# Kernel tuning notes

Hardware: AMD Instinct MI355X
Metric: run time of the kernel (lower is better)

The kernel has to match this reference:

```python
import jax, jax.numpy as jnp
import numpy as np

B = 64  # number of graph pairs in the batch


def gcn_conv(x, W, b, edge_index, n_nodes):
    """PyG GCNConv: add self-loops, symmetric deg^-1/2 normalization, x@W then aggregate."""
    h = x @ W  # [N, out]
    src = jnp.concatenate([edge_index[0], jnp.arange(n_nodes)])
    dst = jnp.concatenate([edge_index[1], jnp.arange(n_nodes)])
    deg = jax.ops.segment_sum(jnp.ones_like(dst, dtype=h.dtype), dst, num_segments=n_nodes)
    dinv = jnp.where(deg > 0, jax.lax.rsqrt(jnp.maximum(deg, 1e-12)), 0.0)
    coef = dinv[src] * dinv[dst]  # [E+N]
    out = jax.ops.segment_sum(coef[:, None] * h[src], dst, num_segments=n_nodes)
    return out + b


def mean_pool(x, batch, num_graphs):
    sums = jax.ops.segment_sum(x, batch, num_segments=num_graphs)
    cnts = jax.ops.segment_sum(jnp.ones((x.shape[0],), x.dtype), batch, num_segments=num_graphs)
    return sums / jnp.maximum(cnts, 1.0)[:, None]


def setup_inputs() -> dict:
    key = jax.random.key(0)
    ks = jax.random.split(key, 32)
    n_prot, e_prot, n_mol, e_mol = 100000, 1600000, 4096, 16384

    def lin(k, fin, fout):
        k1, k2 = jax.random.split(k)
        s = 1.0 / np.sqrt(fin)
        return (jax.random.uniform(k1, (fin, fout), jnp.float32, -s, s),
                jax.random.uniform(k2, (fout,), jnp.float32, -s, s))

    fc1_w, fc1_b = lin(ks[0], 18640, 128)
    fc2_w, fc2_b = lin(ks[1], 128, 128)
    fcm1_w, fcm1_b = lin(ks[2], 21, 64)
    fcm2_w, fcm2_b = lin(ks[3], 64, 64)
    gp1_w, gp1_b = lin(ks[4], 9, 128)
    gp2_w, gp2_b = lin(ks[5], 128, 128)
    gm1_w, gm1_b = lin(ks[6], 9, 128)
    gm2_w, gm2_b = lin(ks[7], 128, 128)
    fcc_w, fcc_b = lin(ks[8], 448, 128)
    out_w, out_b = lin(ks[9], 128, 2)

    return {
        "metadata_prot": jax.random.normal(ks[10], (B, 18640), jnp.float32),
        "metadata_mol": jax.random.normal(ks[11], (B, 21), jnp.float32),
        "x_prot": jax.random.normal(ks[12], (n_prot, 9), jnp.float32),
        "x_mol": jax.random.normal(ks[13], (n_mol, 9), jnp.float32),
        "edge_index_prot": jax.random.randint(ks[14], (2, e_prot), 0, n_prot),
        "batch_vector_prot": jnp.sort(jax.random.randint(ks[15], (n_prot,), 0, B)),
        "edge_index_mol": jax.random.randint(ks[16], (2, e_mol), 0, n_mol),
        "batch_vector_mol": jnp.sort(jax.random.randint(ks[17], (n_mol,), 0, B)),
        "fc1_w": fc1_w, "fc1_b": fc1_b, "fc2_w": fc2_w, "fc2_b": fc2_b,
        "fcm1_w": fcm1_w, "fcm1_b": fcm1_b, "fcm2_w": fcm2_w, "fcm2_b": fcm2_b,
        "gp1_w": gp1_w, "gp1_b": gp1_b, "gp2_w": gp2_w, "gp2_b": gp2_b,
        "gm1_w": gm1_w, "gm1_b": gm1_b, "gm2_w": gm2_w, "gm2_b": gm2_b,
        "fcc_w": fcc_w, "fcc_b": fcc_b, "out_w": out_w, "out_b": out_b,
    }


def reference(metadata_prot, metadata_mol, x_prot, x_mol,
              edge_index_prot, batch_vector_prot, edge_index_mol, batch_vector_mol,
              fc1_w, fc1_b, fc2_w, fc2_b, fcm1_w, fcm1_b, fcm2_w, fcm2_b,
              gp1_w, gp1_b, gp2_w, gp2_b, gm1_w, gm1_b, gm2_w, gm2_b,
              fcc_w, fcc_b, out_w, out_b):
    relu = jax.nn.relu
    mp = relu(relu(metadata_prot @ fc1_w + fc1_b) @ fc2_w + fc2_b)
    mm = relu(relu(metadata_mol @ fcm1_w + fcm1_b) @ fcm2_w + fcm2_b)

    n_prot = x_prot.shape[0]
    hp = relu(gcn_conv(x_prot, gp1_w, gp1_b, edge_index_prot, n_prot))
    hp = relu(gcn_conv(hp, gp2_w, gp2_b, edge_index_prot, n_prot))
    hp = mean_pool(hp, batch_vector_prot, B)

    n_mol = x_mol.shape[0]
    hm = relu(gcn_conv(x_mol, gm1_w, gm1_b, edge_index_mol, n_mol))
    hm = relu(gcn_conv(hm, gm2_w, gm2_b, edge_index_mol, n_mol))
    hm = mean_pool(hm, batch_vector_mol, B)

    combined = jnp.concatenate([mp, mm, hp, hm], axis=1)  # [B, 448]
    combined = relu(combined @ fcc_w + fcc_b)
    return relu(combined @ out_w + out_b)  # [B, 2]
```

## Files before the change

### kernel.cpp

```cpp
#include <hip/hip_runtime.h>

#define CAP 64
#define GB  64
#define FC1K 18640
#define CH 932
#define KS 20
#define NRP 8

typedef __attribute__((ext_vector_type(8))) short bf16x8;
typedef __attribute__((ext_vector_type(4))) float f32x4;

static inline int cdiv(long a, long b){ return (int)((a + b - 1) / b); }

__device__ inline unsigned short pack_bf1(float a) {
  unsigned ua = __float_as_uint(a); ua += 0x7fffu + ((ua >> 16) & 1u);
  return (unsigned short)(ua >> 16);
}
__device__ inline unsigned pack_bf2(float a, float b) {
  unsigned ua = __float_as_uint(a); ua += 0x7fffu + ((ua >> 16) & 1u);
  unsigned ub = __float_as_uint(b); ub += 0x7fffu + ((ub >> 16) & 1u);
  return (ua >> 16) | (ub & 0xffff0000u);
}
__device__ inline float unpack_lo(unsigned short u) { return __uint_as_float(((unsigned)u) << 16); }

__global__ void k_mega(const float* __restrict__ md, const float* __restrict__ fc1w,
                       float* __restrict__ part,
                       const int* __restrict__ ei_m, int EM,
                       int* __restrict__ cnt_m, int* __restrict__ idx_m, int MOLB,
                       const int* __restrict__ bv_p, int NP,
                       const int* __restrict__ bv_m, int NM,
                       float* __restrict__ cntp, float* __restrict__ cntm,
                       const int* __restrict__ ei_p, int EP, int step,
                       int* __restrict__ cnt_p, int* __restrict__ idx_p) {
  __shared__ float smd[64][KS];
  int bid = blockIdx.x;
  int tid = threadIdx.x;

  if (bid < CH) {
    int c = bid;
    int k0 = c * KS;
    for (int t = tid; t < 64 * KS; t += 256) {
      int b = t / KS, k = t % KS;
      smd[b][k] = md[(size_t)b * FC1K + k0 + k];
    }
    __syncthreads();
    int j = tid & 127, bg = tid >> 7;
    float acc[32];
    #pragma unroll
    for (int i = 0; i < 32; i++) acc[i] = 0.f;
    for (int k = 0; k < KS; k++) {
      float w = fc1w[(size_t)(k0 + k) * 128 + j];
      #pragma unroll
      for (int i = 0; i < 32; i++) acc[i] += smd[bg * 32 + i][k] * w;
    }
    float* dst = part + ((size_t)c * 64 + bg * 32) * 128 + j;
    #pragma unroll
    for (int i = 0; i < 32; i++) dst[(size_t)i * 128] = acc[i];
    return;
  }
  bid -= CH;

  if (bid < MOLB) {
    int e = bid * 256 + tid;
    if (e < EM) {
      int s = ei_m[e], d = ei_m[EM + e];
      int c = atomicAdd(&cnt_m[d], 1);
      if (c < CAP) idx_m[d * CAP + c] = s;
    }
    return;
  }
  bid -= MOLB;

  if (bid == 0) {
    if (tid < 128) {
      const int* batch; float* cnt; int n, b;
      if (tid < 64) { batch = bv_p; n = NP; cnt = cntp; b = tid; }
      else          { batch = bv_m; n = NM; cnt = cntm; b = tid - 64; }
      int lo = 0, hi = n;
      while (lo < hi) { int mid = (lo + hi) >> 1; if (batch[mid] < b) lo = mid + 1; else hi = mid; }
      int start = lo;
      lo = 0; hi = n;
      while (lo < hi) { int mid = (lo + hi) >> 1; if (batch[mid] <= b) lo = mid + 1; else hi = mid; }
      cnt[b] = (float)(lo - start);
    }
    return;
  }
  bid -= 1;

  {
    int r = bid & 7;
    int lo = r * step, hi = lo + step; if (hi > NP) hi = NP;
    long eb = (long)(bid >> 3) * 1024 + tid;
    int d0 = -1, d1 = -1, d2 = -1, d3 = -1;
    if (eb       < EP) d0 = ei_p[EP + eb];
    if (eb + 256 < EP) d1 = ei_p[EP + eb + 256];
    if (eb + 512 < EP) d2 = ei_p[EP + eb + 512];
    if (eb + 768 < EP) d3 = ei_p[EP + eb + 768];
    bool a0 = (d0 >= lo) & (d0 < hi);
    bool a1 = (d1 >= lo) & (d1 < hi);
    bool a2 = (d2 >= lo) & (d2 < hi);
    bool a3 = (d3 >= lo) & (d3 < hi);
    int s0 = a0 ? ei_p[eb]       : 0;
    int s1 = a1 ? ei_p[eb + 256] : 0;
    int s2 = a2 ? ei_p[eb + 512] : 0;
    int s3 = a3 ? ei_p[eb + 768] : 0;
    if (a0) { int c = atomicAdd(&cnt_p[d0], 1); if (c < CAP) idx_p[d0 * CAP + c] = s0; }
    if (a1) { int c = atomicAdd(&cnt_p[d1], 1); if (c < CAP) idx_p[d1 * CAP + c] = s1; }
    if (a2) { int c = atomicAdd(&cnt_p[d2], 1); if (c < CAP) idx_p[d2 * CAP + c] = s2; }
    if (a3) { int c = atomicAdd(&cnt_p[d3], 1); if (c < CAP) idx_p[d3 * CAP + c] = s3; }
  }
}

__global__ void k_prep(const float* __restrict__ part, const float* __restrict__ b1,
                       const float* __restrict__ W2, const float* __restrict__ b2,
                       float* __restrict__ mp,
                       const int* __restrict__ cnt_p, const float* __restrict__ x_p,
                       float* __restrict__ dinv_p, unsigned short* __restrict__ xs_p, int np,
                       const int* __restrict__ cnt_m, const float* __restrict__ x_m,
                       float* __restrict__ dinv_m, unsigned short* __restrict__ xs_m, int nm) {
  __shared__ float red[8][128];
  __shared__ float row[128];
  int bid = blockIdx.x, tid = threadIdx.x;
  if (bid < GB) {
    int b = bid;
    int j = tid & 127, kg = tid >> 7;
    float acc = 0.f;
    #pragma unroll 4
    for (int c = kg; c < CH; c += 8) acc += part[((size_t)c * 64 + b) * 128 + j];
    red[kg][j] = acc;
    __syncthreads();
    if (kg == 0) {
      float s = red[0][j] + red[1][j] + red[2][j] + red[3][j]
              + red[4][j] + red[5][j] + red[6][j] + red[7][j];
      row[j] = fmaxf(s + b1[j], 0.f);
    }
    __syncthreads();
    float a2 = 0.f;
    int k0 = kg * 16;
    #pragma unroll
    for (int k = k0; k < k0 + 16; k++) a2 += row[k] * W2[k * 128 + j];
    red[kg][j] = a2;
    __syncthreads();
    if (kg == 0) {
      float s = red[0][j] + red[1][j] + red[2][j] + red[3][j]
              + red[4][j] + red[5][j] + red[6][j] + red[7][j];
      mp[b * 128 + j] = fmaxf(s + b2[j], 0.f);
    }
    return;
  }
  long t = (long)(bid - GB) * 1024 + tid;
  const int* cnt; const float* x; float* dinv; unsigned short* xs; int v, f;
  long tp = (long)np * 16;
  if (t < tp) { v = (int)(t >> 4); f = (int)(t & 15); cnt = cnt_p; x = x_p; dinv = dinv_p; xs = xs_p; }
  else {
    t -= tp;
    if (t >= (long)nm * 16) return;
    v = (int)(t >> 4); f = (int)(t & 15); cnt = cnt_m; x = x_m; dinv = dinv_m; xs = xs_m;
  }
  float d = rsqrtf((float)cnt[v] + 1.0f);
  if (f == 0) dinv[v] = d;
  xs[(size_t)v * 16 + f] = (f < 9) ? pack_bf1(d * x[(size_t)v * 9 + f]) : (unsigned short)0;
}

__global__ void k_gcn1(const unsigned short* __restrict__ xs_p, const float* __restrict__ dinv_p,
                       const int* __restrict__ cnt_p, const int* __restrict__ idx_p,
                       const float* __restrict__ W1p, const float* __restrict__ b1p,
                       const float* __restrict__ W2p, unsigned* __restrict__ hout_p, int np,
                       const unsigned short* __restrict__ xs_m, const float* __restrict__ dinv_m,
                       const int* __restrict__ cnt_m, const int* __restrict__ idx_m,
                       const float* __restrict__ W1m, const float* __restrict__ b1m,
                       const float* __restrict__ W2m, unsigned* __restrict__ hout_m, int nm,
                       int PB) {
  __shared__ float W1s[9 * 128];
  __shared__ float b1s[128];
  __shared__ float axs[16][16];
  __shared__ uint4 As4[256];
  const unsigned short* xs; const float* dinv; const int* cnt; const int* idx;
  const float* W1; const float* b1; const float* W2; unsigned* hout; int n, tile0, gsz;
  if ((int)blockIdx.x < PB) {
    xs = xs_p; dinv = dinv_p; cnt = cnt_p; idx = idx_p;
    W1 = W1p; b1 = b1p; W2 = W2p; hout = hout_p; n = np;
    tile0 = blockIdx.x; gsz = PB;
  } else {
    xs = xs_m; dinv = dinv_m; cnt = cnt_m; idx = idx_m;
    W1 = W1m; b1 = b1m; W2 = W2m; hout = hout_m; n = nm;
    tile0 = blockIdx.x - PB; gsz = gridDim.x - PB;
  }
  int ntiles = (n + 15) >> 4;
  int tid = threadIdx.x;
  int lane = tid & 63;
  int wave = tid >> 6;
  int l15 = lane & 15;
  int lg  = lane >> 4;

  for (int i = tid; i < 9 * 128; i += 256) W1s[i] = W1[i];
  if (tid < 128) b1s[tid] = b1[tid];

  bf16x8 bfrag[2][4];
  #pragma unroll
  for (int ct = 0; ct < 2; ct++) {
    int col = wave * 32 + ct * 16 + l15;
    #pragma unroll
    for (int ks = 0; ks < 4; ks++) {
      #pragma unroll
      for (int j = 0; j < 8; j++) {
        int k = ks * 32 + lg * 8 + j;
        bfrag[ct][ks][j] = (short)pack_bf1(W2[(size_t)k * 128 + col]);
      }
    }
  }
  __syncthreads();

  int r = tid >> 4, c4 = tid & 15;
  for (int tile = tile0; tile < ntiles; tile += gsz) {
    int base = tile * 16;
    int v = base + r;
    float acc = 0.f;
    if (v < n) {
      int deg = cnt[v]; if (deg > CAP) deg = CAP;
      const int* idxv = idx + (size_t)v * CAP;
      acc = unpack_lo(xs[(size_t)v * 16 + c4]);
      int p = 0;
      for (; p + 4 <= deg; p += 4) {
        int s0 = idxv[p], s1 = idxv[p + 1], s2 = idxv[p + 2], s3 = idxv[p + 3];
        float a0 = unpack_lo(xs[(size_t)s0 * 16 + c4]);
        float a1 = unpack_lo(xs[(size_t)s1 * 16 + c4]);
        float a2 = unpack_lo(xs[(size_t)s2 * 16 + c4]);
        float a3 = unpack_lo(xs[(size_t)s3 * 16 + c4]);
        acc += a0; acc += a1; acc += a2; acc += a3;
      }
      for (; p < deg; p++) acc += unpack_lo(xs[(size_t)idxv[p] * 16 + c4]);
      acc *= dinv[v];
    }
    axs[r][c4] = acc;
    __syncthreads();

    float h[8];
    int j0 = c4 * 8;
    #pragma unroll
    for (int jj = 0; jj < 8; jj++) h[jj] = b1s[j0 + jj];
    #pragma unroll
    for (int k = 0; k < 9; k++) {
      float a = axs[r][k];
      #pragma unroll
      for (int jj = 0; jj < 8; jj++) h[jj] += a * W1s[k * 128 + j0 + jj];
    }
    uint4 av;
    av.x = pack_bf2(fmaxf(h[0], 0.f), fmaxf(h[1], 0.f));
    av.y = pack_bf2(fmaxf(h[2], 0.f), fmaxf(h[3], 0.f));
    av.z = pack_bf2(fmaxf(h[4], 0.f), fmaxf(h[5], 0.f));
    av.w = pack_bf2(fmaxf(h[6], 0.f), fmaxf(h[7], 0.f));
    As4[r * 16 + (c4 ^ r)] = av;
    __syncthreads();

    bf16x8 afr[4];
    #pragma unroll
    for (int ks = 0; ks < 4; ks++) {
      uint4 a4 = As4[l15 * 16 + (((ks * 4) + lg) ^ l15)];
      afr[ks] = *(bf16x8*)&a4;
    }

    f32x4 acc0 = {0.f, 0.f, 0.f, 0.f}, acc1 = {0.f, 0.f, 0.f, 0.f};
    #pragma unroll
    for (int ks = 0; ks < 4; ks++) {
      acc0 = __builtin_amdgcn_mfma_f32_16x16x32_bf16(afr[ks], bfrag[0][ks], acc0, 0, 0, 0);
      acc1 = __builtin_amdgcn_mfma_f32_16x16x32_bf16(afr[ks], bfrag[1][ks], acc1, 0, 0, 0);
    }

    #pragma unroll
    for (int reg = 0; reg < 4; reg++) {
      int row = lg * 4 + reg;
      int ov = base + row;
      if (ov < n) {
        float dv = dinv[ov];
        unsigned short* hp16 = (unsigned short*)hout;
        hp16[(size_t)ov * 128 + wave * 32 + l15]      = pack_bf1(dv * acc0[reg]);
        hp16[(size_t)ov * 128 + wave * 32 + 16 + l15] = pack_bf1(dv * acc1[reg]);
      }
    }
    __syncthreads();
  }
}

__global__ void k_gather_bf2(const unsigned* __restrict__ hb_p, const float* __restrict__ dinv_p,
                             const int* __restrict__ cnt_p, const int* __restrict__ idx_p,
                             const float* __restrict__ bias_p, unsigned* __restrict__ out_p, int np,
                             const unsigned* __restrict__ hb_m, const float* __restrict__ dinv_m,
                             const int* __restrict__ cnt_m, const int* __restrict__ idx_m,
                             const float* __restrict__ bias_m, unsigned* __restrict__ out_m, int nm,
                             int PB) {
  const unsigned* hb; const float* dinv; const int* cnt; const int* idx;
  const float* bias; unsigned* out; int n; long t;
  if ((int)blockIdx.x < PB) {
    hb = hb_p; dinv = dinv_p; cnt = cnt_p; idx = idx_p; bias = bias_p; out = out_p; n = np;
    t = (long)blockIdx.x * 256 + threadIdx.x;
  } else {
    hb = hb_m; dinv = dinv_m; cnt = cnt_m; idx = idx_m; bias = bias_m; out = out_m; n = nm;
    t = (long)(blockIdx.x - PB) * 256 + threadIdx.x;
  }
  int v = (int)(t >> 6), f = (int)(t & 63);
  if (v >= n) return;
  float dv = dinv[v];
  int deg = cnt[v]; if (deg > CAP) deg = CAP;
  const int* idxv = idx + (size_t)v * CAP;
  unsigned u = hb[(size_t)v * 64 + f];
  float accL = __uint_as_float(u << 16);
  float accH = __uint_as_float(u & 0xffff0000u);
  int p = 0;
  for (; p + 8 <= deg; p += 8) {
    int s0 = idxv[p], s1 = idxv[p+1], s2 = idxv[p+2], s3 = idxv[p+3];
    int s4 = idxv[p+4], s5 = idxv[p+5], s6 = idxv[p+6], s7 = idxv[p+7];
    unsigned u0 = hb[(size_t)s0 * 64 + f];
    unsigned u1 = hb[(size_t)s1 * 64 + f];
    unsigned u2 = hb[(size_t)s2 * 64 + f];
    unsigned u3 = hb[(size_t)s3 * 64 + f];
    unsigned u4 = hb[(size_t)s4 * 64 + f];
    unsigned u5 = hb[(size_t)s5 * 64 + f];
    unsigned u6 = hb[(size_t)s6 * 64 + f];
    unsigned u7 = hb[(size_t)s7 * 64 + f];
    accL += __uint_as_float(u0 << 16); accH += __uint_as_float(u0 & 0xffff0000u);
    accL += __uint_as_float(u1 << 16); accH += __uint_as_float(u1 & 0xffff0000u);
    accL += __uint_as_float(u2 << 16); accH += __uint_as_float(u2 & 0xffff0000u);
    accL += __uint_as_float(u3 << 16); accH += __uint_as_float(u3 & 0xffff0000u);
    accL += __uint_as_float(u4 << 16); accH += __uint_as_float(u4 & 0xffff0000u);
    accL += __uint_as_float(u5 << 16); accH += __uint_as_float(u5 & 0xffff0000u);
    accL += __uint_as_float(u6 << 16); accH += __uint_as_float(u6 & 0xffff0000u);
    accL += __uint_as_float(u7 << 16); accH += __uint_as_float(u7 & 0xffff0000u);
  }
  for (; p < deg; p++) {
    int s = idxv[p];
    unsigned uu = hb[(size_t)s * 64 + f];
    accL += __uint_as_float(uu << 16); accH += __uint_as_float(uu & 0xffff0000u);
  }
  float2 b2 = *(const float2*)&bias[2 * f];
  float ox = fmaxf(dv * accL + b2.x, 0.f);
  float oy = fmaxf(dv * accH + b2.y, 0.f);
  out[(size_t)v * 64 + f] = pack_bf2(ox, oy);
}

__global__ void k_pool_bf2(const unsigned* __restrict__ h_p, const int* __restrict__ batch_p,
                           float* __restrict__ sums_p, int np,
                           const unsigned* __restrict__ h_m, const int* __restrict__ batch_m,
                           float* __restrict__ sums_m, int nm, int PB) {
  const unsigned* h; const int* batch; float* sums; int n; long v0;
  if ((int)blockIdx.x < PB) {
    h = h_p; batch = batch_p; sums = sums_p; n = np; v0 = (long)blockIdx.x * 64;
  } else {
    h = h_m; batch = batch_m; sums = sums_m; n = nm; v0 = (long)(blockIdx.x - PB) * 64;
  }
  int f = threadIdx.x;
  if (v0 >= n) return;
  long v1 = v0 + 64; if (v1 > n) v1 = n;
  int cur = batch[v0];
  float acc = 0.f;
  for (long v = v0; v < v1; ++v) {
    int bv = batch[v];
    if (bv != cur) { atomicAdd(&sums[cur * 128 + f], acc); acc = 0.f; cur = bv; }
    unsigned u = h[(size_t)v * 64 + (f >> 1)];
    acc += (f & 1) ? __uint_as_float(u & 0xffff0000u) : __uint_as_float(u << 16);
  }
  atomicAdd(&sums[cur * 128 + f], acc);
}

__global__ void k_fcc_final(const float* __restrict__ mp,
                            const float* __restrict__ md_mol,
                            const float* __restrict__ fcm1_w, const float* __restrict__ fcm1_b,
                            const float* __restrict__ fcm2_w, const float* __restrict__ fcm2_b,
                            const float* __restrict__ hpS, const float* __restrict__ hmS,
                            const float* __restrict__ cntp, const float* __restrict__ cntm,
                            const float* __restrict__ W, const float* __restrict__ bias,
                            const float* __restrict__ outw, const float* __restrict__ outb,
                            float* __restrict__ out) {
  __shared__ float row[448];
  __shared__ float mrow[21];
  __shared__ float h1m[64];
  __shared__ float red[8][128];
  __shared__ float frow[128];
  int b = blockIdx.x, tid = threadIdx.x;
  int j = tid & 127, kg = tid >> 7;
  if (tid < 21) mrow[tid] = md_mol[b * 21 + tid];
  if (tid < 128) row[tid] = mp[b * 128 + tid];
  else if (tid >= 192 && tid < 320) row[tid] = hpS[b * 128 + (tid - 192)] / fmaxf(cntp[b], 1.f);
  else if (tid >= 320 && tid < 448) row[tid] = hmS[b * 128 + (tid - 320)] / fmaxf(cntm[b], 1.f);
  __syncthreads();
  if (tid < 64) {
    float a = fcm1_b[tid];
    #pragma unroll 7
    for (int k = 0; k < 21; k++) a += mrow[k] * fcm1_w[k * 64 + tid];
    h1m[tid] = fmaxf(a, 0.f);
  }
  __syncthreads();
  if (tid < 64) {
    float a = fcm2_b[tid];
    #pragma unroll 8
    for (int k = 0; k < 64; k++) a += h1m[k] * fcm2_w[k * 64 + tid];
    row[128 + tid] = fmaxf(a, 0.f);
  }
  __syncthreads();
  float acc = 0.f;
  int k0 = kg * 56;
  #pragma unroll 8
  for (int k = k0; k < k0 + 56; k++) acc += row[k] * W[k * 128 + j];
  red[kg][j] = acc;
  __syncthreads();
  if (kg == 0) {
    float s = red[0][j] + red[1][j] + red[2][j] + red[3][j]
            + red[4][j] + red[5][j] + red[6][j] + red[7][j];
    frow[j] = fmaxf(s + bias[j], 0.f);
  }
  __syncthreads();
  if (tid < 128) {
    int o = tid >> 6, l = tid & 63;
    float p = frow[l] * outw[l * 2 + o] + frow[64 + l] * outw[(64 + l) * 2 + o];
    #pragma unroll
    for (int off = 32; off; off >>= 1) p += __shfl_down(p, off);
    if (l == 0) out[b * 2 + o] = fmaxf(p + outb[o], 0.f);
  }
}

extern "C" void kernel_launch(void* const* d_in, const int* in_sizes, int n_in,
                              void* d_out, int out_size, void* d_ws, size_t ws_size,
                              hipStream_t stream) {
  const float* md_prot = (const float*)d_in[0];
  const float* md_mol  = (const float*)d_in[1];
  const float* x_prot  = (const float*)d_in[2];
  const float* x_mol   = (const float*)d_in[3];
  const int*   ei_p    = (const int*)d_in[4];
  const int*   bv_p    = (const int*)d_in[5];
  const int*   ei_m    = (const int*)d_in[6];
  const int*   bv_m    = (const int*)d_in[7];
  const float* fc1_w = (const float*)d_in[8],  * fc1_b = (const float*)d_in[9];
  const float* fc2_w = (const float*)d_in[10], * fc2_b = (const float*)d_in[11];
  const float* fcm1_w= (const float*)d_in[12], * fcm1_b= (const float*)d_in[13];
  const float* fcm2_w= (const float*)d_in[14], * fcm2_b= (const float*)d_in[15];
  const float* gp1_w = (const float*)d_in[16], * gp1_b = (const float*)d_in[17];
  const float* gp2_w = (const float*)d_in[18], * gp2_b = (const float*)d_in[19];
  const float* gm1_w = (const float*)d_in[20], * gm1_b = (const float*)d_in[21];
  const float* gm2_w = (const float*)d_in[22], * gm2_b = (const float*)d_in[23];
  const float* fcc_w = (const float*)d_in[24], * fcc_b = (const float*)d_in[25];
  const float* out_w = (const float*)d_in[26], * out_b = (const float*)d_in[27];

  const int NP = in_sizes[2] / 9;
  const int EP = in_sizes[4] / 2;
  const int NM = in_sizes[3] / 9;
  const int EM = in_sizes[6] / 2;
  const int MOLB = cdiv(EM, 256);

  char* w = (char*)d_ws;
  size_t off = 0;
  auto take = [&](size_t bytes) -> void* {
    void* p = w + off;
    off = (off + bytes + 255) & ~(size_t)255;
    return p;
  };
  char*     big    = (char*)take((size_t)NP * 128 * 4);
  float*    part   = (float*)big;
  unsigned* hbf_p  = (unsigned*)big;
  unsigned* obf_p  = (unsigned*)(big + (size_t)NP * 64 * 4);
  unsigned short* xs_p = (unsigned short*)take((size_t)NP * 16 * 2);
  int*      idx_p  = (int*)  take((size_t)NP * CAP * 4);
  float*    dinv_p = (float*)take((size_t)NP * 4);
  unsigned short* xs_m = (unsigned short*)take((size_t)NM * 16 * 2);
  unsigned* hbf_m  = (unsigned*)take((size_t)NM * 64 * 4);
  unsigned* obf_m  = (unsigned*)take((size_t)NM * 64 * 4);
  int*      idx_m  = (int*)  take((size_t)NM * CAP * 4);
  float*    dinv_m = (float*)take((size_t)NM * 4);
  float*    mp     = (float*)take(GB * 128 * 4);
  size_t zb_cnt_p = (size_t)NP * 4;
  size_t zb_cnt_m = (size_t)NM * 4;
  size_t zb_hp    = (size_t)GB * 128 * 4;
  size_t zb_hm    = (size_t)GB * 128 * 4;
  size_t zb_cp    = (size_t)GB * 4;
  size_t zb_cm    = (size_t)GB * 4;
  char* zr = (char*)take(zb_cnt_p + zb_cnt_m + zb_hp + zb_hm + zb_cp + zb_cm);
  int*   cnt_p = (int*)zr;
  int*   cnt_m = (int*)(zr + zb_cnt_p);
  float* hp    = (float*)(zr + zb_cnt_p + zb_cnt_m);
  float* hm    = (float*)(zr + zb_cnt_p + zb_cnt_m + zb_hp);
  float* cntp  = (float*)(zr + zb_cnt_p + zb_cnt_m + zb_hp + zb_hm);
  float* cntm  = (float*)(zr + zb_cnt_p + zb_cnt_m + zb_hp + zb_hm + zb_cp);
  (void)ws_size; (void)n_in; (void)out_size;

  hipMemsetAsync(zr, 0, zb_cnt_p + zb_cnt_m + zb_hp + zb_hm + zb_cp + zb_cm, stream);

  {
    int step = cdiv(NP, NRP);
    int PFB  = 8 * cdiv(EP, 1024);
    k_mega<<<CH + MOLB + 1 + PFB, 256, 0, stream>>>(
        md_prot, fc1_w, part,
        ei_m, EM, cnt_m, idx_m, MOLB,
        bv_p, NP, bv_m, NM, cntp, cntm,
        ei_p, EP, step, cnt_p, idx_p);
  }

  k_prep<<<GB + cdiv((long)(NP + NM) * 16, 1024), 1024, 0, stream>>>(
      part, fc1_b, fc2_w, fc2_b, mp,
      cnt_p, x_prot, dinv_p, xs_p, NP,
      cnt_m, x_mol, dinv_m, xs_m, NM);

  k_gcn1<<<2048 + 256, 256, 0, stream>>>(
      xs_p, dinv_p, cnt_p, idx_p, gp1_w, gp1_b, gp2_w, hbf_p, NP,
      xs_m, dinv_m, cnt_m, idx_m, gm1_w, gm1_b, gm2_w, hbf_m, NM, 2048);

  {
    int PBg = cdiv((long)NP * 64, 256);
    k_gather_bf2<<<PBg + cdiv((long)NM * 64, 256), 256, 0, stream>>>(
        hbf_p, dinv_p, cnt_p, idx_p, gp2_b, obf_p, NP,
        hbf_m, dinv_m, cnt_m, idx_m, gm2_b, obf_m, NM, PBg);
  }
  {
    int PBp = cdiv(NP, 64);
    k_pool_bf2<<<PBp + cdiv(NM, 64), 128, 0, stream>>>(
        obf_p, bv_p, hp, NP, obf_m, bv_m, hm, NM, PBp);
  }

  k_fcc_final<<<GB, 1024, 0, stream>>>(mp, md_mol, fcm1_w, fcm1_b, fcm2_w, fcm2_b,
                                       hp, hm, cntp, cntm,
                                       fcc_w, fcc_b, out_w, out_b, (float*)d_out);
}
```

Before: 265.4 us.

## Fuse second GCN gather with mean-pool via per-node atomic accumulation

```diff
diff --git a/kernel.cpp b/kernel.cpp
--- a/kernel.cpp
+++ b/kernel.cpp
@@ -282,20 +282,24 @@
   }
 }
 
-__global__ void k_gather_bf2(const unsigned* __restrict__ hb_p, const float* __restrict__ dinv_p,
-                             const int* __restrict__ cnt_p, const int* __restrict__ idx_p,
-                             const float* __restrict__ bias_p, unsigned* __restrict__ out_p, int np,
-                             const unsigned* __restrict__ hb_m, const float* __restrict__ dinv_m,
-                             const int* __restrict__ cnt_m, const int* __restrict__ idx_m,
-                             const float* __restrict__ bias_m, unsigned* __restrict__ out_m, int nm,
-                             int PB) {
+__global__ void k_gather_pool2(const unsigned* __restrict__ hb_p, const float* __restrict__ dinv_p,
+                               const int* __restrict__ cnt_p, const int* __restrict__ idx_p,
+                               const float* __restrict__ bias_p, const int* __restrict__ batch_p,
+                               float* __restrict__ sums_p, int np,
+                               const unsigned* __restrict__ hb_m, const float* __restrict__ dinv_m,
+                               const int* __restrict__ cnt_m, const int* __restrict__ idx_m,
+                               const float* __restrict__ bias_m, const int* __restrict__ batch_m,
+                               float* __restrict__ sums_m, int nm,
+                               int PB) {
   const unsigned* hb; const float* dinv; const int* cnt; const int* idx;
-  const float* bias; unsigned* out; int n; long t;
+  const float* bias; const int* batch; float* sums; int n; long t;
   if ((int)blockIdx.x < PB) {
-    hb = hb_p; dinv = dinv_p; cnt = cnt_p; idx = idx_p; bias = bias_p; out = out_p; n = np;
+    hb = hb_p; dinv = dinv_p; cnt = cnt_p; idx = idx_p; bias = bias_p;
+    batch = batch_p; sums = sums_p; n = np;
     t = (long)blockIdx.x * 256 + threadIdx.x;
   } else {
-    hb = hb_m; dinv = dinv_m; cnt = cnt_m; idx = idx_m; bias = bias_m; out = out_m; n = nm;
+    hb = hb_m; dinv = dinv_m; cnt = cnt_m; idx = idx_m; bias = bias_m;
+    batch = batch_m; sums = sums_m; n = nm;
     t = (long)(blockIdx.x - PB) * 256 + threadIdx.x;
   }
   int v = (int)(t >> 6), f = (int)(t & 63);
@@ -335,31 +339,9 @@
   float2 b2 = *(const float2*)&bias[2 * f];
   float ox = fmaxf(dv * accL + b2.x, 0.f);
   float oy = fmaxf(dv * accH + b2.y, 0.f);
-  out[(size_t)v * 64 + f] = pack_bf2(ox, oy);
-}
-
-__global__ void k_pool_bf2(const unsigned* __restrict__ h_p, const int* __restrict__ batch_p,
-                           float* __restrict__ sums_p, int np,
-                           const unsigned* __restrict__ h_m, const int* __restrict__ batch_m,
-                           float* __restrict__ sums_m, int nm, int PB) {
-  const unsigned* h; const int* batch; float* sums; int n; long v0;
-  if ((int)blockIdx.x < PB) {
-    h = h_p; batch = batch_p; sums = sums_p; n = np; v0 = (long)blockIdx.x * 64;
-  } else {
-    h = h_m; batch = batch_m; sums = sums_m; n = nm; v0 = (long)(blockIdx.x - PB) * 64;
-  }
-  int f = threadIdx.x;
-  if (v0 >= n) return;
-  long v1 = v0 + 64; if (v1 > n) v1 = n;
-  int cur = batch[v0];
-  float acc = 0.f;
-  for (long v = v0; v < v1; ++v) {
-    int bv = batch[v];
-    if (bv != cur) { atomicAdd(&sums[cur * 128 + f], acc); acc = 0.f; cur = bv; }
-    unsigned u = h[(size_t)v * 64 + (f >> 1)];
-    acc += (f & 1) ? __uint_as_float(u & 0xffff0000u) : __uint_as_float(u << 16);
-  }
-  atomicAdd(&sums[cur * 128 + f], acc);
+  int g = batch[v];
+  atomicAdd(&sums[g * 128 + 2 * f],     ox);
+  atomicAdd(&sums[g * 128 + 2 * f + 1], oy);
 }
 
 __global__ void k_fcc_final(const float* __restrict__ mp,
@@ -456,13 +438,11 @@
   char*     big    = (char*)take((size_t)NP * 128 * 4);
   float*    part   = (float*)big;
   unsigned* hbf_p  = (unsigned*)big;
-  unsigned* obf_p  = (unsigned*)(big + (size_t)NP * 64 * 4);
   unsigned short* xs_p = (unsigned short*)take((size_t)NP * 16 * 2);
   int*      idx_p  = (int*)  take((size_t)NP * CAP * 4);
   float*    dinv_p = (float*)take((size_t)NP * 4);
   unsigned short* xs_m = (unsigned short*)take((size_t)NM * 16 * 2);
   unsigned* hbf_m  = (unsigned*)take((size_t)NM * 64 * 4);
-  unsigned* obf_m  = (unsigned*)take((size_t)NM * 64 * 4);
   int*      idx_m  = (int*)  take((size_t)NM * CAP * 4);
   float*    dinv_m = (float*)take((size_t)NM * 4);
   float*    mp     = (float*)take(GB * 128 * 4);
@@ -504,14 +484,9 @@
 
   {
     int PBg = cdiv((long)NP * 64, 256);
-    k_gather_bf2<<<PBg + cdiv((long)NM * 64, 256), 256, 0, stream>>>(
-        hbf_p, dinv_p, cnt_p, idx_p, gp2_b, obf_p, NP,
-        hbf_m, dinv_m, cnt_m, idx_m, gm2_b, obf_m, NM, PBg);
-  }
-  {
-    int PBp = cdiv(NP, 64);
-    k_pool_bf2<<<PBp + cdiv(NM, 64), 128, 0, stream>>>(
-        obf_p, bv_p, hp, NP, obf_m, bv_m, hm, NM, PBp);
+    k_gather_pool2<<<PBg + cdiv((long)NM * 64, 256), 256, 0, stream>>>(
+        hbf_p, dinv_p, cnt_p, idx_p, gp2_b, bv_p, hp, NP,
+        hbf_m, dinv_m, cnt_m, idx_m, gm2_b, bv_m, hm, NM, PBg);
   }
 
   k_fcc_final<<<GB, 1024, 0, stream>>>(mp, md_mol, fcm1_w, fcm1_b, fcm2_w, fcm2_b,
```

After: 503.6 us. 89.8% more time.
